# Kernel tuning notes

Hardware: AMD Instinct MI355X
Metric: run time of the kernel (lower is better)

## Reference

```python
import jax, jax.numpy as jnp
import numpy as np

B, S, E, H = 4, 1024, 1024, 16
D = E // H          # head_dim = 64
F = 4 * E           # mlp inner = 4096
EPS = 1e-5


def _layernorm(x, scale, bias):
    mu = jnp.mean(x, axis=-1, keepdims=True)
    var = jnp.var(x, axis=-1, keepdims=True)
    return (x - mu) * jax.lax.rsqrt(var + EPS) * scale + bias


def setup_inputs() -> dict:
    key = jax.random.key(0)
    ks = jax.random.split(key, 8)
    std = 0.02
    return {
        "hidden_states": jax.random.normal(ks[0], (B, S, E), jnp.float32),
        "ln1_scale": jnp.ones((E,), jnp.float32),
        "ln1_bias": jnp.zeros((E,), jnp.float32),
        # Conv1D kernels stored as (out_features, in_features), applied as x @ k.T
        "w_attn": jax.random.normal(ks[1], (3 * E, E), jnp.float32) * std,
        "b_attn": jnp.zeros((3 * E,), jnp.float32),
        "w_proj": jax.random.normal(ks[2], (E, E), jnp.float32) * std,
        "b_proj": jnp.zeros((E,), jnp.float32),
        "ln2_scale": jnp.ones((E,), jnp.float32),
        "ln2_bias": jnp.zeros((E,), jnp.float32),
        "w_fc": jax.random.normal(ks[3], (F, E), jnp.float32) * std,
        "b_fc": jnp.zeros((F,), jnp.float32),
        "w_proj2": jax.random.normal(ks[4], (E, F), jnp.float32) * std,
        "b_proj2": jnp.zeros((E,), jnp.float32),
    }


def reference(hidden_states, ln1_scale, ln1_bias, w_attn, b_attn, w_proj, b_proj,
              ln2_scale, ln2_bias, w_fc, b_fc, w_proj2, b_proj2):
    x = hidden_states
    # --- attention sub-block ---
    h = _layernorm(x, ln1_scale, ln1_bias)
    qkv = h @ w_attn.T + b_attn                      # [B,S,3E]
    q, k, v = jnp.split(qkv, 3, axis=2)
    q = q.reshape(B, S, H, D) / jnp.sqrt(jnp.float32(D))
    k = k.reshape(B, S, H, D)
    v = v.reshape(B, S, H, D)
    # NOTE: source sets attention_bias = None, so NO causal mask is applied.
    logits = jnp.einsum("bqhd,bkhd->bhqk", q, k)     # [B,H,S,S]
    attn = jax.nn.softmax(logits, axis=-1)
    o = jnp.einsum("bhqk,bkhd->bqhd", attn, v).reshape(B, S, E)
    o = o @ w_proj.T + b_proj
    x = x + o
    # --- mlp sub-block ---
    h = _layernorm(x, ln2_scale, ln2_bias)
    m = jax.nn.gelu(h @ w_fc.T + b_fc, approximate=True)  # gelu_new
    m = m @ w_proj2.T + b_proj2
    return x + m
```

## Files before the change

### kernel.cpp

```cpp
#include <hip/hip_runtime.h>

#define DEV __device__ __forceinline__

using bf16x8 = __attribute__((ext_vector_type(8))) __bf16;
using f32x4  = __attribute__((ext_vector_type(4))) float;
typedef unsigned int u32;
typedef unsigned short u16;
typedef unsigned long long u64;

static constexpr int Bb = 4, Ss = 1024, Ee = 1024, Hh = 16, Dd = 64, Ff = 4096;
static constexpr int Mm = Bb * Ss;

DEV u16 f2bf(float f) {
  union { float f; u32 u; } v; v.f = f;
  u32 r = v.u + 0x7fffu + ((v.u >> 16) & 1u);
  return (u16)(r >> 16);
}

DEV void gload16(const void* g, void* lds) {
  __builtin_amdgcn_global_load_lds(
      (const __attribute__((address_space(1))) void*)(u64)g,
      (__attribute__((address_space(3))) void*)(u32)(u64)lds,
      16, 0, 0);
}

DEV float gelu_tanh(float x) {
  float x3 = x * x * x;
  float t  = tanhf(0.7978845608028654f * (x + 0.044715f * x3));
  return 0.5f * x * (1.0f + t);
}

DEV int swz(int row, int col) { return row * 64 + (col ^ ((row & 7) << 3)); }

DEV f32x4 MFMA(bf16x8 a, bf16x8 b, f32x4 c) {
  return __builtin_amdgcn_mfma_f32_16x16x32_bf16(a, b, c, 0, 0, 0);
}

__global__ __launch_bounds__(256) void cvt_bf16(const float* __restrict__ in,
                                                u16* __restrict__ out, int n) {
  int i = (blockIdx.x * 256 + threadIdx.x) * 8;
  if (i >= n) return;
  float4 a = *(const float4*)(in + i);
  float4 b = *(const float4*)(in + i + 4);
  uint4 o;
  o.x = (u32)f2bf(a.x) | ((u32)f2bf(a.y) << 16);
  o.y = (u32)f2bf(a.z) | ((u32)f2bf(a.w) << 16);
  o.z = (u32)f2bf(b.x) | ((u32)f2bf(b.y) << 16);
  o.w = (u32)f2bf(b.z) | ((u32)f2bf(b.w) << 16);
  *(uint4*)(out + i) = o;
}

__global__ __launch_bounds__(256) void ln_kernel(const float* __restrict__ x,
                                                 const float* __restrict__ scale,
                                                 const float* __restrict__ bias,
                                                 u16* __restrict__ h) {
  const int row = blockIdx.x, tid = threadIdx.x;
  const float4 v = ((const float4*)(x + (size_t)row * Ee))[tid];
  float s  = v.x + v.y + v.z + v.w;
  float ss = v.x * v.x + v.y * v.y + v.z * v.z + v.w * v.w;
  for (int m = 1; m < 64; m <<= 1) {
    s  += __shfl_xor(s, m, 64);
    ss += __shfl_xor(ss, m, 64);
  }
  __shared__ float red[8];
  const int w = tid >> 6, ln = tid & 63;
  if (ln == 0) { red[w * 2] = s; red[w * 2 + 1] = ss; }
  __syncthreads();
  s  = red[0] + red[2] + red[4] + red[6];
  ss = red[1] + red[3] + red[5] + red[7];
  const float mu   = s * (1.0f / Ee);
  const float var  = ss * (1.0f / Ee) - mu * mu;
  const float rstd = rsqrtf(var + 1e-5f);
  const float4 sc = ((const float4*)scale)[tid];
  const float4 bi = ((const float4*)bias)[tid];
  ushort4 o;
  o.x = f2bf((v.x - mu) * rstd * sc.x + bi.x);
  o.y = f2bf((v.y - mu) * rstd * sc.y + bi.y);
  o.z = f2bf((v.z - mu) * rstd * sc.z + bi.z);
  o.w = f2bf((v.w - mu) * rstd * sc.w + bi.w);
  ((ushort4*)(h + (size_t)row * Ee))[tid] = o;
}

template <int EPI, int AM, int AN>
__global__ __launch_bounds__(256, 5) void gemm3(
    const u16* __restrict__ A, const u16* __restrict__ Bw,
    const float* __restrict__ bias, const float* __restrict__ resid,
    float* __restrict__ outf, u16* __restrict__ outb,
    u16* __restrict__ q, u16* __restrict__ k, u16* __restrict__ v,
    int N, int K) {
  constexpr int BM = AM * 32, BN = AN * 32;
  constexpr int GA = BM / 64, GB = BN / 64;
  __shared__ u16 As[2][BM * 32];
  __shared__ u16 Bs[2][BN * 32];
  const int tid = threadIdx.x;
  const int w = tid >> 6, ln = tid & 63;
  const int lr = ln & 15, lg = ln >> 4;
  const int wr = w >> 1, wc = w & 1;

  const int nwg = gridDim.x * gridDim.y;
  const int bid = blockIdx.y * gridDim.x + blockIdx.x;
  const int sid = (bid & 7) * (nwg >> 3) + (bid >> 3);
  const int bx = sid % gridDim.x, by = sid / gridDim.x;
  const int tm = by * BM, tn = bx * BN;

  f32x4 acc[AM][AN];
  f32x4 zero4 = {0.f, 0.f, 0.f, 0.f};
#pragma unroll
  for (int i = 0; i < AM; ++i)
#pragma unroll
    for (int j = 0; j < AN; ++j) acc[i][j] = zero4;

  const int r0 = tid >> 2;
  const int cs = ((tid & 3) ^ (r0 & 3)) * 8;
  const u16* aP[GA];
  const u16* bP[GB];
#pragma unroll
  for (int i = 0; i < GA; ++i) aP[i] = A + (size_t)(tm + r0 + i * 64) * K + cs;
#pragma unroll
  for (int i = 0; i < GB; ++i) bP[i] = Bw + (size_t)(tn + r0 + i * 64) * K + cs;

  auto STAGE = [&](int buf, int k0) {
#pragma unroll
    for (int i = 0; i < GA; ++i)
      gload16(aP[i] + k0, &As[buf][(tid + i * 256) * 8]);
#pragma unroll
    for (int i = 0; i < GB; ++i)
      gload16(bP[i] + k0, &Bs[buf][(tid + i * 256) * 8]);
  };

  const int fsl = (lg ^ (lr & 3)) << 3;
  const int nt = K >> 5;
  STAGE(0, 0);
  asm volatile("s_waitcnt vmcnt(0)" ::: "memory");
  __builtin_amdgcn_s_barrier();

  for (int t = 0; t < nt; ++t) {
    if (t + 1 < nt) STAGE((t + 1) & 1, (t + 1) << 5);
    const u16* Ab = &As[t & 1][0];
    const u16* Bbuf = &Bs[t & 1][0];
    bf16x8 af[AM], bf[AN];
#pragma unroll
    for (int mi = 0; mi < AM; ++mi)
      af[mi] = *(const bf16x8*)&Ab[(wr * AM * 16 + mi * 16 + lr) * 32 + fsl];
#pragma unroll
    for (int ni = 0; ni < AN; ++ni)
      bf[ni] = *(const bf16x8*)&Bbuf[(wc * AN * 16 + ni * 16 + lr) * 32 + fsl];
#pragma unroll
    for (int mi = 0; mi < AM; ++mi)
#pragma unroll
      for (int ni = 0; ni < AN; ++ni)
        acc[mi][ni] = MFMA(af[mi], bf[ni], acc[mi][ni]);
    asm volatile("s_waitcnt vmcnt(0)" ::: "memory");
    __builtin_amdgcn_s_barrier();
  }

#pragma unroll
  for (int mi = 0; mi < AM; ++mi) {
#pragma unroll
    for (int ni = 0; ni < AN; ++ni) {
      const int gc = tn + wc * AN * 16 + ni * 16 + lr;
#pragma unroll
      for (int j = 0; j < 4; ++j) {
        const int gr = tm + wr * AM * 16 + mi * 16 + lg * 4 + j;
        float val = acc[mi][ni][j] + bias[gc];
        if constexpr (EPI == 0) {
          const int which = gc >> 10, hh = (gc >> 6) & 15, dd = gc & 63;
          const int bb2 = gr >> 10, ss2 = gr & 1023;
          const size_t dst = ((size_t)(bb2 * 16 + hh) * 1024 + ss2) * 64 + dd;
          if (which == 0)      q[dst] = f2bf(val * 0.125f);
          else if (which == 1) k[dst] = f2bf(val);
          else                 v[dst] = f2bf(val);
        } else if constexpr (EPI == 1) {
          const size_t idx = (size_t)gr * N + gc;
          outf[idx] = val + resid[idx];
        } else {
          outb[(size_t)gr * N + gc] = f2bf(gelu_tanh(val));
        }
      }
    }
  }
}

__global__ __launch_bounds__(256) void attn_kernel(const u16* __restrict__ qg,
                                                   const u16* __restrict__ kg,
                                                   const u16* __restrict__ vg,
                                                   u16* __restrict__ ao) {
  __shared__ u16 Qs[64 * 64], Ks[64 * 64], Vt[64 * 64], Ps[64 * 64];
  const int tid = threadIdx.x;
  const int w = tid >> 6, ln = tid & 63;
  const int lr = ln & 15, lg = ln >> 4;
  const int bh = blockIdx.y;
  const int q0 = blockIdx.x * 64;
  const size_t head = (size_t)bh * (Ss * Dd);

  {
    const u16* src = qg + head + (size_t)q0 * Dd;
#pragma unroll
    for (int i = 0; i < 2; ++i) {
      const int gi = i * 256 + tid, row = gi >> 3, g = gi & 7;
      *(uint4*)&Qs[row * 64 + ((g ^ (row & 7)) << 3)] = *(const uint4*)(src + gi * 8);
    }
  }

  f32x4 zero4 = {0.f, 0.f, 0.f, 0.f};
  f32x4 acc_o[4] = {zero4, zero4, zero4, zero4};
  float mrow[4] = {-1e30f, -1e30f, -1e30f, -1e30f};
  float lrow[4] = {0.f, 0.f, 0.f, 0.f};

  for (int kt = 0; kt < 16; ++kt) {
    __syncthreads();
    const u16* ksrc = kg + head + (size_t)kt * 64 * Dd;
    const u16* vsrc = vg + head + (size_t)kt * 64 * Dd;
#pragma unroll
    for (int i = 0; i < 2; ++i) {
      const int gi = i * 256 + tid, row = gi >> 3, g = gi & 7;
      *(uint4*)&Ks[row * 64 + ((g ^ (row & 7)) << 3)] = *(const uint4*)(ksrc + gi * 8);
    }
#pragma unroll
    for (int i = 0; i < 2; ++i) {
      const int kv = i * 32 + (tid >> 3), d0 = (tid & 7) * 8;
      uint4 dv = *(const uint4*)(vsrc + (size_t)kv * Dd + d0);
      const u16* pv = (const u16*)&dv;
#pragma unroll
      for (int j = 0; j < 8; ++j) {
        const int dd = d0 + j;
        Vt[dd * 64 + (((kv >> 3) ^ (dd & 7)) << 3) + (kv & 7)] = pv[j];
      }
    }
    __syncthreads();

    bf16x8 aq[2];
#pragma unroll
    for (int kk = 0; kk < 2; ++kk)
      aq[kk] = *(const bf16x8*)&Qs[swz(w * 16 + lr, kk * 32 + lg * 8)];
    f32x4 sa[4];
#pragma unroll
    for (int kf = 0; kf < 4; ++kf) {
      f32x4 s = zero4;
#pragma unroll
      for (int kk = 0; kk < 2; ++kk) {
        bf16x8 bk = *(const bf16x8*)&Ks[swz(kf * 16 + lr, kk * 32 + lg * 8)];
        s = MFMA(aq[kk], bk, s);
      }
      sa[kf] = s;
    }

#pragma unroll
    for (int j = 0; j < 4; ++j) {
      float mx = fmaxf(fmaxf(sa[0][j], sa[1][j]), fmaxf(sa[2][j], sa[3][j]));
      mx = fmaxf(mx, __shfl_xor(mx, 1, 64));
      mx = fmaxf(mx, __shfl_xor(mx, 2, 64));
      mx = fmaxf(mx, __shfl_xor(mx, 4, 64));
      mx = fmaxf(mx, __shfl_xor(mx, 8, 64));
      const float nm = fmaxf(mrow[j], mx);
      const float corr = __expf(mrow[j] - nm);
      mrow[j] = nm;
      float ssum = 0.f;
#pragma unroll
      for (int kf = 0; kf < 4; ++kf) {
        const float p = __expf(sa[kf][j] - nm);
        sa[kf][j] = p;
        ssum += p;
      }
      ssum += __shfl_xor(ssum, 1, 64);
      ssum += __shfl_xor(ssum, 2, 64);
      ssum += __shfl_xor(ssum, 4, 64);
      ssum += __shfl_xor(ssum, 8, 64);
      lrow[j] = lrow[j] * corr + ssum;
#pragma unroll
      for (int df = 0; df < 4; ++df) acc_o[df][j] *= corr;
    }

#pragma unroll
    for (int kf = 0; kf < 4; ++kf)
#pragma unroll
      for (int j = 0; j < 4; ++j)
        Ps[swz(w * 16 + lg * 4 + j, kf * 16 + lr)] = f2bf(sa[kf][j]);

    __syncthreads();

    bf16x8 ap[2];
#pragma unroll
    for (int kk = 0; kk < 2; ++kk)
      ap[kk] = *(const bf16x8*)&Ps[swz(w * 16 + lr, kk * 32 + lg * 8)];
#pragma unroll
    for (int df = 0; df < 4; ++df) {
#pragma unroll
      for (int kk = 0; kk < 2; ++kk) {
        bf16x8 bv = *(const bf16x8*)&Vt[swz(df * 16 + lr, kk * 32 + lg * 8)];
        acc_o[df] = MFMA(ap[kk], bv, acc_o[df]);
      }
    }
  }

  const int b = bh >> 4, h = bh & 15;
#pragma unroll
  for (int df = 0; df < 4; ++df) {
#pragma unroll
    for (int j = 0; j < 4; ++j) {
      const int srow = q0 + w * 16 + lg * 4 + j;
      const int e = h * 64 + df * 16 + lr;
      ao[((size_t)b * Ss + srow) * Ee + e] = f2bf(acc_o[df][j] / lrow[j]);
    }
  }
}

extern "C" void kernel_launch(void* const* d_in, const int* in_sizes, int n_in,
                              void* d_out, int out_size, void* d_ws, size_t ws_size,
                              hipStream_t stream) {
  const float* x      = (const float*)d_in[0];
  const float* ln1_s  = (const float*)d_in[1];
  const float* ln1_b  = (const float*)d_in[2];
  const float* w_attn = (const float*)d_in[3];
  const float* b_attn = (const float*)d_in[4];
  const float* w_proj = (const float*)d_in[5];
  const float* b_proj = (const float*)d_in[6];
  const float* ln2_s  = (const float*)d_in[7];
  const float* ln2_b  = (const float*)d_in[8];
  const float* w_fc   = (const float*)d_in[9];
  const float* b_fc   = (const float*)d_in[10];
  const float* w_proj2= (const float*)d_in[11];
  const float* b_proj2= (const float*)d_in[12];
  float* out = (float*)d_out;

  char* base = (char*)d_ws;
  size_t off = 0;
  auto alloc = [&](size_t bytes) { char* p = base + off; off += bytes; return p; };
  u16* wA   = (u16*)alloc((size_t)3 * Ee * Ee * 2);
  u16* wP   = (u16*)alloc((size_t)Ee * Ee * 2);
  u16* wF   = (u16*)alloc((size_t)Ff * Ee * 2);
  u16* wP2  = (u16*)alloc((size_t)Ee * Ff * 2);
  u16* h1   = (u16*)alloc((size_t)Mm * Ee * 2);
  u16* qws  = (u16*)alloc((size_t)Mm * Ee * 2);
  u16* kws  = (u16*)alloc((size_t)Mm * Ee * 2);
  u16* vws  = (u16*)alloc((size_t)Mm * Ee * 2);
  u16* aws  = (u16*)alloc((size_t)Mm * Ee * 2);
  float* x1 = (float*)alloc((size_t)Mm * Ee * 4);
  u16* mfc  = qws;

  cvt_bf16<<<3 * Ee * Ee / 2048, 256, 0, stream>>>(w_attn, wA, 3 * Ee * Ee);
  cvt_bf16<<<Ee * Ee / 2048, 256, 0, stream>>>(w_proj, wP, Ee * Ee);
  cvt_bf16<<<Ff * Ee / 2048, 256, 0, stream>>>(w_fc, wF, Ff * Ee);
  cvt_bf16<<<Ee * Ff / 2048, 256, 0, stream>>>(w_proj2, wP2, Ee * Ff);

  ln_kernel<<<Mm, 256, 0, stream>>>(x, ln1_s, ln1_b, h1);
  gemm3<0, 4, 2><<<dim3(48, 32), 256, 0, stream>>>(h1, wA, b_attn, nullptr,
                                                   nullptr, nullptr, qws, kws, vws,
                                                   3 * Ee, Ee);
  attn_kernel<<<dim3(16, 64), 256, 0, stream>>>(qws, kws, vws, aws);
  gemm3<1, 2, 2><<<dim3(16, 64), 256, 0, stream>>>(aws, wP, b_proj, x,
                                                   x1, nullptr, nullptr, nullptr, nullptr,
                                                   Ee, Ee);
  ln_kernel<<<Mm, 256, 0, stream>>>(x1, ln2_s, ln2_b, h1);
  gemm3<2, 4, 2><<<dim3(64, 32), 256, 0, stream>>>(h1, wF, b_fc, nullptr,
                                                   nullptr, mfc, nullptr, nullptr, nullptr,
                                                   Ff, Ee);
  gemm3<1, 2, 2><<<dim3(16, 64), 256, 0, stream>>>(mfc, wP2, b_proj2, x1,
                                                   out, nullptr, nullptr, nullptr, nullptr,
                                                   Ee, Ff);
}
```

Baseline: 307.1 us.

## Add 128x128 triple-buffered residual GEMM, remap attention grid, tweak occupancy

Adds a new residual-epilogue GEMM kernel with 128x128 tiles, a 4x4 MFMA accumulator per wave and a three-stage LDS pipeline using direct global-to-LDS loads. It replaces the small-tile 64x64 GEMMs for the attention output projection and the MLP down projection, raising data reuse per tile. The attention kernel moves to a 1D grid with heads interleaved across blocks and rotates the V-transpose store order to reduce LDS bank conflicts. The remaining gemm3 gets a higher occupancy hint. The output projection grid shrinks to 256 blocks, which may underfill the GPU's compute units.

```diff
diff --git a/kernel.cpp b/kernel.cpp
--- a/kernel.cpp
+++ b/kernel.cpp
@@ -82,10 +82,10 @@
 }
 
 template <int EPI, int AM, int AN>
-__global__ __launch_bounds__(256, 5) void gemm3(
+__global__ __launch_bounds__(256, 6) void gemm3(
     const u16* __restrict__ A, const u16* __restrict__ Bw,
-    const float* __restrict__ bias, const float* __restrict__ resid,
-    float* __restrict__ outf, u16* __restrict__ outb,
+    const float* __restrict__ bias,
+    u16* __restrict__ outb,
     u16* __restrict__ q, u16* __restrict__ k, u16* __restrict__ v,
     int N, int K) {
   constexpr int BM = AM * 32, BN = AN * 32;
@@ -170,9 +170,6 @@
           if (which == 0)      q[dst] = f2bf(val * 0.125f);
           else if (which == 1) k[dst] = f2bf(val);
           else                 v[dst] = f2bf(val);
-        } else if constexpr (EPI == 1) {
-          const size_t idx = (size_t)gr * N + gc;
-          outf[idx] = val + resid[idx];
         } else {
           outb[(size_t)gr * N + gc] = f2bf(gelu_tanh(val));
         }
@@ -181,17 +178,111 @@
   }
 }
 
-__global__ __launch_bounds__(256) void attn_kernel(const u16* __restrict__ qg,
-                                                   const u16* __restrict__ kg,
-                                                   const u16* __restrict__ vg,
-                                                   u16* __restrict__ ao) {
+__global__ __launch_bounds__(256, 3) void gemm2r(
+    const u16* __restrict__ A, const u16* __restrict__ Bw,
+    const float* __restrict__ bias, const float* __restrict__ resid,
+    float* __restrict__ outf, int N, int K) {
+  __shared__ u16 As[3][128 * 32];
+  __shared__ u16 Bs[3][128 * 32];
+  const int tid = threadIdx.x;
+  const int w = tid >> 6, ln = tid & 63;
+  const int lr = ln & 15, lg = ln >> 4;
+
+  const int nwg = gridDim.x * gridDim.y;
+  const int bid = blockIdx.y * gridDim.x + blockIdx.x;
+  const int sid = (bid & 7) * (nwg >> 3) + (bid >> 3);
+  const int bx = sid % gridDim.x, by = sid / gridDim.x;
+  const int tm = by * 128, tn = bx * 128;
+  const int wr = (w >> 1) * 64, wc = (w & 1) * 64;
+
+  f32x4 zero4 = {0.f, 0.f, 0.f, 0.f};
+  f32x4 acc[4][4];
+#pragma unroll
+  for (int i = 0; i < 4; ++i)
+#pragma unroll
+    for (int j = 0; j < 4; ++j) acc[i][j] = zero4;
+
+  const int r0 = tid >> 2, sl = tid & 3;
+  const int cs = (sl ^ (r0 & 3)) * 8;
+  const u16* aP0 = A  + (size_t)(tm + r0) * K + cs;
+  const u16* aP1 = A  + (size_t)(tm + 64 + r0) * K + cs;
+  const u16* bP0 = Bw + (size_t)(tn + r0) * K + cs;
+  const u16* bP1 = Bw + (size_t)(tn + 64 + r0) * K + cs;
+
+  auto STAGE = [&](int buf, int k0) {
+    gload16(aP0 + k0, &As[buf][tid * 8]);
+    gload16(aP1 + k0, &As[buf][(256 + tid) * 8]);
+    gload16(bP0 + k0, &Bs[buf][tid * 8]);
+    gload16(bP1 + k0, &Bs[buf][(256 + tid) * 8]);
+  };
+
+  const int nt = K >> 5;
+  STAGE(0, 0);
+  STAGE(1, 32);
+  asm volatile("s_waitcnt vmcnt(4)" ::: "memory");
+  __builtin_amdgcn_s_barrier();
+  __builtin_amdgcn_sched_barrier(0);
+
+  for (int t = 0; t < nt; ++t) {
+    const int cur = t % 3;
+    const bool more = (t + 2) < nt;
+    if (more) STAGE((t + 2) % 3, (t + 2) << 5);
+
+    bf16x8 af[4], bb[4];
+#pragma unroll
+    for (int mi = 0; mi < 4; ++mi) {
+      const int row = wr + mi * 16 + lr;
+      af[mi] = *(const bf16x8*)&As[cur][row * 32 + ((lg ^ (row & 3)) << 3)];
+    }
+#pragma unroll
+    for (int ni = 0; ni < 4; ++ni) {
+      const int row = wc + ni * 16 + lr;
+      bb[ni] = *(const bf16x8*)&Bs[cur][row * 32 + ((lg ^ (row & 3)) << 3)];
+    }
+    __builtin_amdgcn_s_setprio(1);
+#pragma unroll
+    for (int mi = 0; mi < 4; ++mi)
+#pragma unroll
+      for (int ni = 0; ni < 4; ++ni)
+        acc[mi][ni] = MFMA(af[mi], bb[ni], acc[mi][ni]);
+    __builtin_amdgcn_s_setprio(0);
+    __builtin_amdgcn_sched_barrier(0);
+    if (more) asm volatile("s_waitcnt vmcnt(4)" ::: "memory");
+    else      asm volatile("s_waitcnt vmcnt(0)" ::: "memory");
+    __builtin_amdgcn_s_barrier();
+    __builtin_amdgcn_sched_barrier(0);
+  }
+
+#pragma unroll
+  for (int mi = 0; mi < 4; ++mi) {
+#pragma unroll
+    for (int ni = 0; ni < 4; ++ni) {
+      const int gc = tn + wc + ni * 16 + lr;
+#pragma unroll
+      for (int j = 0; j < 4; ++j) {
+        const int gr = tm + wr + mi * 16 + lg * 4 + j;
+        const size_t idx = (size_t)gr * N + gc;
+        outf[idx] = acc[mi][ni][j] + bias[gc] + resid[idx];
+      }
+    }
+  }
+}
+
+__global__ __launch_bounds__(256) void attn4(const u16* __restrict__ qg,
+                                             const u16* __restrict__ kg,
+                                             const u16* __restrict__ vg,
+                                             u16* __restrict__ ao) {
   __shared__ u16 Qs[64 * 64], Ks[64 * 64], Vt[64 * 64], Ps[64 * 64];
   const int tid = threadIdx.x;
   const int w = tid >> 6, ln = tid & 63;
   const int lr = ln & 15, lg = ln >> 4;
-  const int bh = blockIdx.y;
-  const int q0 = blockIdx.x * 64;
+
+  const int bid = blockIdx.x;
+  const int bh = (bid & 7) * 8 + ((bid >> 3) & 7);
+  const int q0 = (bid >> 6) * 64;
   const size_t head = (size_t)bh * (Ss * Dd);
+
+  const int dsel = tid & 7, d0 = dsel * 8;
 
   {
     const u16* src = qg + head + (size_t)q0 * Dd;
@@ -218,13 +309,14 @@
     }
 #pragma unroll
     for (int i = 0; i < 2; ++i) {
-      const int kv = i * 32 + (tid >> 3), d0 = (tid & 7) * 8;
+      const int kv = i * 32 + (tid >> 3);
       uint4 dv = *(const uint4*)(vsrc + (size_t)kv * Dd + d0);
       const u16* pv = (const u16*)&dv;
 #pragma unroll
-      for (int j = 0; j < 8; ++j) {
+      for (int jj = 0; jj < 8; ++jj) {
+        const int j = (jj + dsel) & 7;
         const int dd = d0 + j;
-        Vt[dd * 64 + (((kv >> 3) ^ (dd & 7)) << 3) + (kv & 7)] = pv[j];
+        Vt[dd * 64 + (kv & 7) + (((kv >> 3) ^ (dd & 7)) << 3)] = pv[j];
       }
     }
     __syncthreads();
@@ -344,18 +436,14 @@
   cvt_bf16<<<Ee * Ff / 2048, 256, 0, stream>>>(w_proj2, wP2, Ee * Ff);
 
   ln_kernel<<<Mm, 256, 0, stream>>>(x, ln1_s, ln1_b, h1);
-  gemm3<0, 4, 2><<<dim3(48, 32), 256, 0, stream>>>(h1, wA, b_attn, nullptr,
-                                                   nullptr, nullptr, qws, kws, vws,
+  gemm3<0, 4, 2><<<dim3(48, 32), 256, 0, stream>>>(h1, wA, b_attn,
+                                                   nullptr, qws, kws, vws,
                                                    3 * Ee, Ee);
-  attn_kernel<<<dim3(16, 64), 256, 0, stream>>>(qws, kws, vws, aws);
-  gemm3<1, 2, 2><<<dim3(16, 64), 256, 0, stream>>>(aws, wP, b_proj, x,
-                                                   x1, nullptr, nullptr, nullptr, nullptr,
-                                                   Ee, Ee);
+  attn4<<<1024, 256, 0, stream>>>(qws, kws, vws, aws);
+  gemm2r<<<dim3(8, 32), 256, 0, stream>>>(aws, wP, b_proj, x, x1, Ee, Ee);
   ln_kernel<<<Mm, 256, 0, stream>>>(x1, ln2_s, ln2_b, h1);
-  gemm3<2, 4, 2><<<dim3(64, 32), 256, 0, stream>>>(h1, wF, b_fc, nullptr,
-                                                   nullptr, mfc, nullptr, nullptr, nullptr,
+  gemm3<2, 4, 2><<<dim3(64, 32), 256, 0, stream>>>(h1, wF, b_fc,
+                                                   mfc, nullptr, nullptr, nullptr,
                                                    Ff, Ee);
-  gemm3<1, 2, 2><<<dim3(16, 64), 256, 0, stream>>>(mfc, wP2, b_proj2, x1,
-                                                   out, nullptr, nullptr, nullptr, nullptr,
-                                                   Ee, Ff);
-}
+  gemm2r<<<dim3(8, 32), 256, 0, stream>>>(mfc, wP2, b_proj2, x1, out, Ee, Ff);
+}
```

Result: no change. 307.9 us (+0.3%).
